# Optimization experiments

Measured on AMD Instinct MI355X. Metric: run time of the kernel, lower is better.

The kernel has to match this reference:

```python
import jax, jax.numpy as jnp
import numpy as np

N = 100000
E = 1600000
IN_DIM, HID, OUT = 512, 128, 16


def setup_inputs() -> dict:
    key = jax.random.key(0)
    ks = jax.random.split(key, 8)
    x = jax.random.normal(ks[0], (N, IN_DIM), dtype=jnp.float32)
    edge_index = jax.random.randint(ks[1], (2, E), 0, N, dtype=jnp.int64)
    # GCNConv params (Glorot-ish scale) and Linear head
    W1 = jax.random.normal(ks[2], (IN_DIM, HID), dtype=jnp.float32) / np.sqrt(IN_DIM)
    b1 = jnp.zeros((HID,), dtype=jnp.float32)
    W2 = jax.random.normal(ks[3], (HID, HID), dtype=jnp.float32) / np.sqrt(HID)
    b2 = jnp.zeros((HID,), dtype=jnp.float32)
    Wl = jax.random.normal(ks[4], (HID, OUT), dtype=jnp.float32) / np.sqrt(HID)
    bl = jnp.zeros((OUT,), dtype=jnp.float32)
    return {"x": x, "edge_index": edge_index, "W1": W1, "b1": b1,
            "W2": W2, "b2": b2, "Wl": Wl, "bl": bl}


def _gcn_conv(x, W, b, src, dst, deg_inv_sqrt, deg_inv):
    # h = x @ W ; out[dst] += norm * h[src]; self-loop adds h[i]/deg[i]
    h = x @ W                                           # [N, D]
    norm = deg_inv_sqrt[src] * deg_inv_sqrt[dst]        # [E]
    msgs = h[src] * norm[:, None]                       # [E, D] gather
    agg = jax.ops.segment_sum(msgs, dst, num_segments=x.shape[0])  # scatter
    agg = agg + h * deg_inv[:, None]                    # self-loop term
    return agg + b


def reference(x, edge_index, W1, b1, W2, b2, Wl, bl):
    src, dst = edge_index[0], edge_index[1]
    n = x.shape[0]
    ones = jnp.ones(src.shape[0], dtype=x.dtype)
    # degree with self-loops (PyG gcn_norm counts in-degree at target + 1)
    deg = jax.ops.segment_sum(ones, dst, num_segments=n) + 1.0
    deg_inv_sqrt = jax.lax.rsqrt(deg)
    deg_inv = 1.0 / deg

    h = _gcn_conv(x, W1, b1, src, dst, deg_inv_sqrt, deg_inv)
    h = jax.nn.relu(h)
    # dropout: inference mode (training=False) -> identity
    h = _gcn_conv(h, W2, b2, src, dst, deg_inv_sqrt, deg_inv)
    embeddings = jax.nn.relu(h)
    out = embeddings @ Wl + bl
    return out, embeddings
```

## Files before the change

kernel.cpp:

```cpp
#include <hip/hip_runtime.h>

#define NN 100000
#define EE 1600000
#define IND 512
#define HIDD 128
#define OUTD 16
#define DEG_BLKS 128
#define GEMM_BLKS 1563

typedef __bf16 bf16x8 __attribute__((ext_vector_type(8)));
typedef float f32x4 __attribute__((ext_vector_type(4)));

__device__ __forceinline__ ushort f2bf(float f) {
    union { float f; uint u; } v; v.f = f;
    uint r = v.u + 0x7FFFu + ((v.u >> 16) & 1u);
    return (ushort)(r >> 16);
}

__device__ __forceinline__ uint pk2bf(float a, float b) {
    __bf16 x = (__bf16)a, y = (__bf16)b;
    ushort ux = *(ushort*)&x, uy = *(ushort*)&y;
    return (uint)ux | ((uint)uy << 16);
}

#define GLDS16(src, dst)                                              \
    __builtin_amdgcn_global_load_lds(                                 \
        (const __attribute__((address_space(1))) void*)(src),         \
        (__attribute__((address_space(3))) void*)(dst), 16, 0, 0)

__global__ void k_prep(const float* __restrict__ W1, const float* __restrict__ W2,
                       ushort* __restrict__ Wt1, ushort* __restrict__ Wt2) {
    int b = blockIdx.x, tid = threadIdx.x;
    if (b < 256) {
        int i = b * 256 + tid;
        int k = i >> 7, n = i & 127;
        Wt1[n * 512 + k] = f2bf(W1[i]);
    } else {
        int i = (b - 256) * 256 + tid;
        int k = i >> 7, n = i & 127;
        Wt2[n * 128 + k] = f2bf(W2[i]);
    }
}

__global__ void k_scan_local(const int* __restrict__ deg, int* __restrict__ incl,
                             int* __restrict__ bsum) {
    __shared__ int s[256];
    int tid = threadIdx.x;
    int i = blockIdx.x * 256 + tid;
    int v = (i < NN) ? deg[i] : 0;
    s[tid] = v;
    __syncthreads();
    for (int off = 1; off < 256; off <<= 1) {
        int t = (tid >= off) ? s[tid - off] : 0;
        __syncthreads();
        s[tid] += t;
        __syncthreads();
    }
    if (i < NN) incl[i] = s[tid];
    if (tid == 255) bsum[blockIdx.x] = s[255];
}

__global__ void k_scan_bsum(const int* __restrict__ bsum, int* __restrict__ boff, int n) {
    __shared__ int s[512];
    int tid = threadIdx.x;
    int v = (tid < n) ? bsum[tid] : 0;
    s[tid] = v;
    __syncthreads();
    for (int off = 1; off < 512; off <<= 1) {
        int t = (tid >= off) ? s[tid - off] : 0;
        __syncthreads();
        s[tid] += t;
        __syncthreads();
    }
    if (tid < n) boff[tid] = s[tid] - v;
}

__global__ void k_scan_final(const int* __restrict__ incl, const int* __restrict__ deg,
                             const int* __restrict__ boff, int* __restrict__ rs,
                             int* __restrict__ cursor, float* __restrict__ dis,
                             float* __restrict__ dinv) {
    int i = blockIdx.x * 256 + threadIdx.x;
    if (i < NN) {
        int d = deg[i];
        int v = incl[i] + boff[i >> 8];
        int start = v - d;
        rs[i] = start;
        cursor[i] = start;
        if (i == NN - 1) rs[NN] = v;
        float df = (float)(d + 1);
        dis[i] = rsqrtf(df);
        dinv[i] = 1.0f / df;
    }
}

__global__ void k_fill(const int* __restrict__ src, const int* __restrict__ dst,
                       const float* __restrict__ dis, int* __restrict__ cursor,
                       int2* __restrict__ ew) {
    int i = blockIdx.x * blockDim.x + threadIdx.x;
    int stride = gridDim.x * blockDim.x;
    for (; i < EE; i += stride) {
        int d = dst[i];
        int s = src[i];
        int pos = atomicAdd(&cursor[d], 1);
        ew[pos] = make_int2(s, __float_as_int(dis[s] * dis[d]));
    }
}

template <int K, bool AFP32>
__device__ __forceinline__ void gemm_body(const void* __restrict__ Ap,
                                          const ushort* __restrict__ Wt,
                                          ushort* __restrict__ C, int M, int blk) {
    constexpr int NT = K / 32;
    constexpr int ABYTES = AFP32 ? 64 * 32 * 4 : 64 * 32 * 2;
    constexpr int WBYTES = 128 * 32 * 2;
    __shared__ char smem[2 * (ABYTES + WBYTES)];

    int tid = threadIdx.x;
    int row0 = blk * 64;
    int wid = tid >> 6, lane = tid & 63;
    int wm = wid * 16;
    int lm = lane & 15, lk8 = (lane >> 4) * 8;

    const float* Af = (const float*)Ap;
    const ushort* Ab16 = (const ushort*)Ap;

    f32x4 acc[8];
#pragma unroll
    for (int q = 0; q < 8; q++) acc[q] = (f32x4){0.f, 0.f, 0.f, 0.f};

    auto stage = [&](int bi, int k0) {
        char* Abase = smem + bi * ABYTES;
        char* Wbase = smem + 2 * ABYTES + bi * WBYTES;
        if (AFP32) {
#pragma unroll
            for (int j = 0; j < 2; j++) {
                int c = wid * 2 + j;
                int rp = c * 8 + (lane >> 3);
                int sl = (lane & 7) ^ (rp & 7);
                int gr2 = row0 + rp; if (gr2 >= M) gr2 = M - 1;
                GLDS16(Af + (size_t)gr2 * K + k0 + sl * 4, Abase + c * 1024);
            }
        } else {
            int c = wid;
            int rp = c * 16 + (lane >> 2);
            int sl = (lane & 3) ^ (rp & 3);
            int gr2 = row0 + rp; if (gr2 >= M) gr2 = M - 1;
            GLDS16(Ab16 + (size_t)gr2 * K + k0 + sl * 8, Abase + c * 1024);
        }
#pragma unroll
        for (int j = 0; j < 2; j++) {
            int c = wid * 2 + j;
            int rp = c * 16 + (lane >> 2);
            int sl = (lane & 3) ^ (rp & 3);
            GLDS16(Wt + (size_t)rp * K + k0 + sl * 8, Wbase + c * 1024);
        }
    };

    stage(0, 0);

    int cur = 0;
    for (int t = 0; t < NT; t++) {
        if (t + 1 < NT) {
            stage((t + 1) & 1, (t + 1) * 32);
            if (AFP32) asm volatile("s_waitcnt vmcnt(4)" ::: "memory");
            else       asm volatile("s_waitcnt vmcnt(3)" ::: "memory");
        } else {
            asm volatile("s_waitcnt vmcnt(0)" ::: "memory");
        }
        __builtin_amdgcn_s_barrier();

        char* Abase = smem + cur * ABYTES;
        char* Wbase = smem + 2 * ABYTES + cur * WBYTES;
        bf16x8 xf, wf[8];
        if (AFP32) {
            int r_ = wm + lm;
            int s0 = lk8 >> 2;
            f32x4 a0 = *(const f32x4*)(Abase + r_ * 128 + (((s0)     ^ (r_ & 7)) << 4));
            f32x4 a1 = *(const f32x4*)(Abase + r_ * 128 + (((s0 + 1) ^ (r_ & 7)) << 4));
            uint4 u;
            u.x = pk2bf(a0[0], a0[1]);
            u.y = pk2bf(a0[2], a0[3]);
            u.z = pk2bf(a1[0], a1[1]);
            u.w = pk2bf(a1[2], a1[3]);
            xf = *(bf16x8*)&u;
        } else {
            int r_ = wm + lm;
            int s = lk8 >> 3;
            uint4 u = *(const uint4*)(Abase + r_ * 64 + ((s ^ (r_ & 3)) << 4));
            xf = *(bf16x8*)&u;
        }
#pragma unroll
        for (int q = 0; q < 8; q++) {
            int n_ = q * 16 + lm;
            int s = lk8 >> 3;
            uint4 u = *(const uint4*)(Wbase + n_ * 64 + ((s ^ (n_ & 3)) << 4));
            wf[q] = *(bf16x8*)&u;
        }
#pragma unroll
        for (int q = 0; q < 8; q++)
            acc[q] = __builtin_amdgcn_mfma_f32_16x16x32_bf16(wf[q], xf, acc[q], 0, 0, 0);

        asm volatile("" ::: "memory");
        __builtin_amdgcn_s_barrier();
        cur ^= 1;
    }

    int cn4 = (lane >> 4) * 4;
    int m = row0 + wm + lm;
    if (m < M) {
#pragma unroll
        for (int q = 0; q < 8; q++) {
            int n = q * 16 + cn4;
            uint2 o;
            o.x = (uint)f2bf(acc[q][0]) | ((uint)f2bf(acc[q][1]) << 16);
            o.y = (uint)f2bf(acc[q][2]) | ((uint)f2bf(acc[q][3]) << 16);
            *(uint2*)(C + (size_t)m * 128 + n) = o;
        }
    }
}

__global__ __launch_bounds__(256, 5) void k_mega1(const float* __restrict__ x,
                                                  const ushort* __restrict__ Wt1,
                                                  ushort* __restrict__ C,
                                                  const int* __restrict__ dst,
                                                  int* __restrict__ deg) {
    if (blockIdx.x < DEG_BLKS) {
        int i = blockIdx.x * 256 + threadIdx.x;
        int stride = DEG_BLKS * 256;
        for (; i < EE; i += stride) atomicAdd(&deg[dst[i]], 1);
    } else {
        gemm_body<IND, true>(x, Wt1, C, NN, blockIdx.x - DEG_BLKS);
    }
}

__global__ __launch_bounds__(256, 6) void k_gemm2(const ushort* __restrict__ A,
                                                  const ushort* __restrict__ Wt,
                                                  ushort* __restrict__ C) {
    gemm_body<HIDD, false>(A, Wt, C, NN, blockIdx.x);
}

template <bool OUTF32>
__global__ __launch_bounds__(256) void k_agg(const ushort* __restrict__ h,
                                             const int* __restrict__ rs,
                                             const int2* __restrict__ ew,
                                             const float* __restrict__ dinv,
                                             const float* __restrict__ bias,
                                             void* __restrict__ yv) {
    int node = blockIdx.x * 4 + (threadIdx.x >> 6);
    int lane = threadIdx.x & 63;
    if (node >= NN) return;
    int half = lane >> 5, c = lane & 31;
    const uint2* h64 = (const uint2*)h;

    float acc0 = 0.f, acc1 = 0.f, acc2 = 0.f, acc3 = 0.f;
    if (half == 0) {
        float dv = dinv[node];
        uint2 sv = h64[(size_t)node * 32 + c];
        acc0 = __uint_as_float(sv.x << 16) * dv;
        acc1 = __uint_as_float(sv.x & 0xffff0000u) * dv;
        acc2 = __uint_as_float(sv.y << 16) * dv;
        acc3 = __uint_as_float(sv.y & 0xffff0000u) * dv;
    }

    int e = rs[node], e1 = rs[node + 1];

#define EL(i) int2 p##i = ew[e + 2 * i + half]; \
              uint2 g##i = h64[(size_t)(uint)p##i.x * 32 + c];
#define EA(i) { float w##i = __int_as_float(p##i.y); \
    acc0 += w##i * __uint_as_float(g##i.x << 16); \
    acc1 += w##i * __uint_as_float(g##i.x & 0xffff0000u); \
    acc2 += w##i * __uint_as_float(g##i.y << 16); \
    acc3 += w##i * __uint_as_float(g##i.y & 0xffff0000u); }

    for (; e + 16 <= e1; e += 16) {
        EL(0) EL(1) EL(2) EL(3) EL(4) EL(5) EL(6) EL(7)
        EA(0) EA(1) EA(2) EA(3) EA(4) EA(5) EA(6) EA(7)
    }
    for (; e + 4 <= e1; e += 4) {
        EL(0) EL(1)
        EA(0) EA(1)
    }
    if (e + 2 <= e1) {
        EL(0)
        EA(0)
        e += 2;
    }
    if (e < e1 && half == 0) {
        int2 p = ew[e];
        uint2 g = h64[(size_t)(uint)p.x * 32 + c];
        float w = __int_as_float(p.y);
        acc0 += w * __uint_as_float(g.x << 16);
        acc1 += w * __uint_as_float(g.x & 0xffff0000u);
        acc2 += w * __uint_as_float(g.y << 16);
        acc3 += w * __uint_as_float(g.y & 0xffff0000u);
    }
#undef EL
#undef EA

    acc0 += __shfl_xor(acc0, 32, 64);
    acc1 += __shfl_xor(acc1, 32, 64);
    acc2 += __shfl_xor(acc2, 32, 64);
    acc3 += __shfl_xor(acc3, 32, 64);

    if (half == 0) {
        float4 bv = *(const float4*)(bias + c * 4);
        acc0 = fmaxf(acc0 + bv.x, 0.f);
        acc1 = fmaxf(acc1 + bv.y, 0.f);
        acc2 = fmaxf(acc2 + bv.z, 0.f);
        acc3 = fmaxf(acc3 + bv.w, 0.f);
        if (OUTF32) {
            *(float4*)((float*)yv + (size_t)node * 128 + c * 4) =
                make_float4(acc0, acc1, acc2, acc3);
        } else {
            uint2 o;
            o.x = (uint)f2bf(acc0) | ((uint)f2bf(acc1) << 16);
            o.y = (uint)f2bf(acc2) | ((uint)f2bf(acc3) << 16);
            *(uint2*)((ushort*)yv + (size_t)node * 128 + c * 4) = o;
        }
    }
}

__global__ __launch_bounds__(256) void k_out(const float* __restrict__ emb,
                                             const float* __restrict__ Wl,
                                             const float* __restrict__ bl,
                                             float* __restrict__ out) {
    __shared__ float wl_s[128 * 16];
    __shared__ float es[16][129];
    int tid = threadIdx.x;
    int row0 = blockIdx.x * 16;
#pragma unroll
    for (int p = 0; p < 8; p++) wl_s[p * 256 + tid] = Wl[p * 256 + tid];
#pragma unroll
    for (int p = 0; p < 8; p++) {
        int idx = p * 256 + tid;
        int r = idx >> 7, c = idx & 127;
        int gr = row0 + r;
        es[r][c] = (gr < NN) ? emb[(size_t)gr * 128 + c] : 0.0f;
    }
    __syncthreads();
    int r = tid >> 4, o = tid & 15;
    float acc = bl[o];
#pragma unroll
    for (int k = 0; k < 128; k++) acc += es[r][k] * wl_s[k * 16 + o];
    int gr = row0 + r;
    if (gr < NN) out[(size_t)gr * 16 + o] = acc;
}

extern "C" void kernel_launch(void* const* d_in, const int* in_sizes, int n_in,
                              void* d_out, int out_size, void* d_ws, size_t ws_size,
                              hipStream_t stream) {
    const float* x  = (const float*)d_in[0];
    const int* ei   = (const int*)d_in[1];
    const float* W1 = (const float*)d_in[2];
    const float* b1 = (const float*)d_in[3];
    const float* W2 = (const float*)d_in[4];
    const float* b2 = (const float*)d_in[5];
    const float* Wl = (const float*)d_in[6];
    const float* bl = (const float*)d_in[7];
    const int* src = ei;
    const int* dst = ei + EE;

    float* outp = (float*)d_out;
    float* emb  = outp + (size_t)NN * OUTD;

    int2* ew    = (int2*)d_ws;
    ushort* h_a = (ushort*)(ew + EE);
    ushort* h_b = h_a + (size_t)NN * 128;
    ushort* Wt1 = h_b + (size_t)NN * 128;
    ushort* Wt2 = Wt1 + 128 * 512;
    int* deg    = (int*)(Wt2 + 128 * 128);
    float* dis  = (float*)(deg + NN);
    float* dinv = dis + NN;
    int* incl   = (int*)(dinv + NN);
    int* rs     = incl + NN;
    int* cursor = rs + NN + 8;
    int* bsum   = cursor + NN;
    int* boff   = bsum + 512;

    const int NB_N = (NN + 255) / 256;

    hipMemsetAsync(deg, 0, (size_t)NN * sizeof(int), stream);
    k_prep<<<320, 256, 0, stream>>>(W1, W2, Wt1, Wt2);
    k_mega1<<<DEG_BLKS + GEMM_BLKS, 256, 0, stream>>>(x, Wt1, h_a, dst, deg);
    k_scan_local<<<NB_N, 256, 0, stream>>>(deg, incl, bsum);
    k_scan_bsum<<<1, 512, 0, stream>>>(bsum, boff, NB_N);
    k_scan_final<<<NB_N, 256, 0, stream>>>(incl, deg, boff, rs, cursor, dis, dinv);
    k_fill<<<2048, 256, 0, stream>>>(src, dst, dis, cursor, ew);

    k_agg<false><<<(NN + 3) / 4, 256, 0, stream>>>(h_a, rs, ew, dinv, b1, h_b);
    k_gemm2<<<GEMM_BLKS, 256, 0, stream>>>(h_b, Wt2, h_a);
    k_agg<true><<<(NN + 3) / 4, 256, 0, stream>>>(h_a, rs, ew, dinv, b2, emb);
    k_out<<<(NN + 15) / 16, 256, 0, stream>>>(emb, Wl, bl, outp);
}
```

Measured before the change: 374.2 us.

## Record per-edge slot from degree atomics to drop fill-phase atomics

The degree-count atomicAdd now returns each edge's slot within its destination bucket, which is stored in a new per-edge pos array. The CSR fill kernel then computes each edge's location as rs[d]+pos[i] with no atomics, and the cursor array is removed. The degree counting is also spread across every GEMM block (1024 edges each) instead of 128 dedicated blocks. In exchange it adds an extra E-sized int write and read, and puts atomic latency in front of the GEMM in every block.

```diff
diff --git a/kernel.cpp b/kernel.cpp
--- a/kernel.cpp
+++ b/kernel.cpp
@@ -5,7 +5,6 @@
 #define IND 512
 #define HIDD 128
 #define OUTD 16
-#define DEG_BLKS 128
 #define GEMM_BLKS 1563
 
 typedef __bf16 bf16x8 __attribute__((ext_vector_type(8)));
@@ -77,15 +76,12 @@
 
 __global__ void k_scan_final(const int* __restrict__ incl, const int* __restrict__ deg,
                              const int* __restrict__ boff, int* __restrict__ rs,
-                             int* __restrict__ cursor, float* __restrict__ dis,
-                             float* __restrict__ dinv) {
+                             float* __restrict__ dis, float* __restrict__ dinv) {
     int i = blockIdx.x * 256 + threadIdx.x;
     if (i < NN) {
         int d = deg[i];
         int v = incl[i] + boff[i >> 8];
-        int start = v - d;
-        rs[i] = start;
-        cursor[i] = start;
+        rs[i] = v - d;
         if (i == NN - 1) rs[NN] = v;
         float df = (float)(d + 1);
         dis[i] = rsqrtf(df);
@@ -94,15 +90,14 @@
 }
 
 __global__ void k_fill(const int* __restrict__ src, const int* __restrict__ dst,
-                       const float* __restrict__ dis, int* __restrict__ cursor,
-                       int2* __restrict__ ew) {
+                       const int* __restrict__ pos, const int* __restrict__ rs,
+                       const float* __restrict__ dis, int2* __restrict__ ew) {
     int i = blockIdx.x * blockDim.x + threadIdx.x;
     int stride = gridDim.x * blockDim.x;
     for (; i < EE; i += stride) {
         int d = dst[i];
         int s = src[i];
-        int pos = atomicAdd(&cursor[d], 1);
-        ew[pos] = make_int2(s, __float_as_int(dis[s] * dis[d]));
+        ew[rs[d] + pos[i]] = make_int2(s, __float_as_int(dis[s] * dis[d]));
     }
 }
 
@@ -223,14 +218,19 @@
                                                   const ushort* __restrict__ Wt1,
                                                   ushort* __restrict__ C,
                                                   const int* __restrict__ dst,
-                                                  int* __restrict__ deg) {
-    if (blockIdx.x < DEG_BLKS) {
-        int i = blockIdx.x * 256 + threadIdx.x;
-        int stride = DEG_BLKS * 256;
-        for (; i < EE; i += stride) atomicAdd(&deg[dst[i]], 1);
-    } else {
-        gemm_body<IND, true>(x, Wt1, C, NN, blockIdx.x - DEG_BLKS);
-    }
+                                                  int* __restrict__ deg,
+                                                  int* __restrict__ pos) {
+    int tid = threadIdx.x;
+    int base = blockIdx.x * 1024;
+#pragma unroll
+    for (int j = 0; j < 4; j++) {
+        int i = base + j * 256 + tid;
+        if (i < EE) {
+            int d = dst[i];
+            pos[i] = atomicAdd(&deg[d], 1);
+        }
+    }
+    gemm_body<IND, true>(x, Wt1, C, NN, blockIdx.x);
 }
 
 __global__ __launch_bounds__(256, 6) void k_gemm2(const ushort* __restrict__ A,
@@ -364,7 +364,8 @@
     float* emb  = outp + (size_t)NN * OUTD;
 
     int2* ew    = (int2*)d_ws;
-    ushort* h_a = (ushort*)(ew + EE);
+    int* pos    = (int*)(ew + EE);
+    ushort* h_a = (ushort*)(pos + EE);
     ushort* h_b = h_a + (size_t)NN * 128;
     ushort* Wt1 = h_b + (size_t)NN * 128;
     ushort* Wt2 = Wt1 + 128 * 512;
@@ -373,19 +374,18 @@
     float* dinv = dis + NN;
     int* incl   = (int*)(dinv + NN);
     int* rs     = incl + NN;
-    int* cursor = rs + NN + 8;
-    int* bsum   = cursor + NN;
+    int* bsum   = rs + NN + 8;
     int* boff   = bsum + 512;
 
     const int NB_N = (NN + 255) / 256;
 
     hipMemsetAsync(deg, 0, (size_t)NN * sizeof(int), stream);
     k_prep<<<320, 256, 0, stream>>>(W1, W2, Wt1, Wt2);
-    k_mega1<<<DEG_BLKS + GEMM_BLKS, 256, 0, stream>>>(x, Wt1, h_a, dst, deg);
+    k_mega1<<<GEMM_BLKS, 256, 0, stream>>>(x, Wt1, h_a, dst, deg, pos);
     k_scan_local<<<NB_N, 256, 0, stream>>>(deg, incl, bsum);
     k_scan_bsum<<<1, 512, 0, stream>>>(bsum, boff, NB_N);
-    k_scan_final<<<NB_N, 256, 0, stream>>>(incl, deg, boff, rs, cursor, dis, dinv);
-    k_fill<<<2048, 256, 0, stream>>>(src, dst, dis, cursor, ew);
+    k_scan_final<<<NB_N, 256, 0, stream>>>(incl, deg, boff, rs, dis, dinv);
+    k_fill<<<2048, 256, 0, stream>>>(src, dst, pos, rs, dis, ew);
 
     k_agg<false><<<(NN + 3) / 4, 256, 0, stream>>>(h_a, rs, ew, dinv, b1, h_b);
     k_gemm2<<<GEMM_BLKS, 256, 0, stream>>>(h_b, Wt2, h_a);
```

Result: no change. 370.1 us (-1.1%).
